# Performance work log

Measured on AMD Instinct MI355X. Metric: run time of the kernel, lower is better.

The kernel has to match this reference:

```python
import jax, jax.numpy as jnp
import numpy as np

NUM_HEADS = 8
EPS = 1e-5


def _dwconv_cpe(x, w, b, H, W):
    # x: [B,N,C]; depthwise 3x3 conv positional encoding with residual
    B, N, C = x.shape
    f = x.transpose(0, 2, 1).reshape(B, C, H, W)
    f = jax.lax.conv_general_dilated(
        f, w, window_strides=(1, 1), padding='SAME',
        feature_group_count=C, dimension_numbers=('NCHW', 'OIHW', 'NCHW'))
    f = f + b[None, :, None, None]
    return x + f.reshape(B, C, N).transpose(0, 2, 1)


def _layernorm(x, g, b):
    mu = jnp.mean(x, axis=-1, keepdims=True)
    var = jnp.mean(jnp.square(x - mu), axis=-1, keepdims=True)
    return (x - mu) * jax.lax.rsqrt(var + EPS) * g + b


def _channel_attn(x, source, q_w, kv_w, proj_w, proj_b):
    B, N, C = x.shape
    h = NUM_HEADS
    d = C // h
    scale = d ** -0.5
    q = (x @ q_w).reshape(B, N, h, d).transpose(0, 2, 1, 3)          # [B,h,N,d]
    kv = (source @ kv_w).reshape(B, N, 2, h, d).transpose(2, 0, 3, 1, 4)
    k = kv[0] * scale                                                # [B,h,N,d]
    v = kv[1]                                                        # [B,h,N,d]
    # channel cross-covariance: [B,h,d,d], softmax over last channel dim
    attn = jax.nn.softmax(jnp.einsum('bhnd,bhne->bhde', k, v), axis=-1)
    out = jnp.einsum('bhde,bhne->bhnd', attn, q)                     # [B,h,N,d]
    out = out.transpose(0, 2, 1, 3).reshape(B, N, C)
    return out @ proj_w + proj_b


def _forward(x, source, H, W, cpe0_w, cpe0_b, cpe1_w, cpe1_b,
             norm1_g, norm1_b, q_w, kv_w, proj_w, proj_b,
             norm2_g, norm2_b, fc1_w, fc1_b, fc2_w, fc2_b):
    x = _dwconv_cpe(x, cpe0_w, cpe0_b, H, W)
    source = _dwconv_cpe(source, cpe0_w, cpe0_b, H, W)  # cpe[0] shared, per source
    x = _layernorm(x, norm1_g, norm1_b)
    source = _layernorm(source, norm1_g, norm1_b)
    cur = _channel_attn(x, source, q_w, kv_w, proj_w, proj_b)
    x = x + cur  # residual on the normalized x (as in the original code)
    x = _dwconv_cpe(x, cpe1_w, cpe1_b, H, W)
    h = _layernorm(x, norm2_g, norm2_b)
    h = jax.nn.gelu(h @ fc1_w + fc1_b, approximate=False) @ fc2_w + fc2_b
    return x + h


def setup_inputs() -> dict:
    key = jax.random.key(0)
    ks = jax.random.split(key, 16)
    B, H, W, C = 8, 64, 64, 384
    N = H * W
    Ch = int(C * 4.0)
    s = 0.02
    return {
        'x': jax.random.normal(ks[0], (B, N, C), jnp.float32),
        'source': jax.random.normal(ks[1], (B, N, C), jnp.float32),
        'H': H, 'W': W,
        'cpe0_w': jax.random.normal(ks[2], (C, 1, 3, 3), jnp.float32) * s,
        'cpe0_b': jnp.zeros((C,), jnp.float32),
        'cpe1_w': jax.random.normal(ks[3], (C, 1, 3, 3), jnp.float32) * s,
        'cpe1_b': jnp.zeros((C,), jnp.float32),
        'norm1_g': jnp.ones((C,), jnp.float32),
        'norm1_b': jnp.zeros((C,), jnp.float32),
        'q_w': jax.random.normal(ks[4], (C, C), jnp.float32) * s,
        'kv_w': jax.random.normal(ks[5], (C, 2 * C), jnp.float32) * s,
        'proj_w': jax.random.normal(ks[6], (C, C), jnp.float32) * s,
        'proj_b': jnp.zeros((C,), jnp.float32),
        'norm2_g': jnp.ones((C,), jnp.float32),
        'norm2_b': jnp.zeros((C,), jnp.float32),
        'fc1_w': jax.random.normal(ks[7], (C, Ch), jnp.float32) * s,
        'fc1_b': jnp.zeros((Ch,), jnp.float32),
        'fc2_w': jax.random.normal(ks[8], (Ch, C), jnp.float32) * s,
        'fc2_b': jnp.zeros((C,), jnp.float32),
    }


def reference(x, source, H, W, cpe0_w, cpe0_b, cpe1_w, cpe1_b,
              norm1_g, norm1_b, q_w, kv_w, proj_w, proj_b,
              norm2_g, norm2_b, fc1_w, fc1_b, fc2_w, fc2_b):
    return _forward(x, source, H, W, cpe0_w, cpe0_b, cpe1_w, cpe1_b,
                    norm1_g, norm1_b, q_w, kv_w, proj_w, proj_b,
                    norm2_g, norm2_b, fc1_w, fc1_b, fc2_w, fc2_b)
```

## Files before the change

kernel.cpp:

```cpp
#include <hip/hip_runtime.h>
#include <hip/hip_bf16.h>
#include <math.h>

typedef __hip_bfloat16 bf16;
typedef unsigned short u16t;
typedef __bf16 bfx8 __attribute__((ext_vector_type(8)));
typedef float fx4 __attribute__((ext_vector_type(4)));
typedef unsigned short usx8 __attribute__((ext_vector_type(8)));

constexpr int Bq = 8, Hh = 64, Ww = 64, Nn = 4096, Cc = 384, NH = 8, CH = 1536;
constexpr int Mrows = Bq * Nn;
constexpr int NS = 4;
constexpr int NSP = 6;
constexpr float EPSC = 1e-5f;
constexpr float SCALE = 0.14433756729740643f;

__device__ __forceinline__ float toF(bf16 v) { return __bfloat162float(v); }

__device__ __forceinline__ float ldFlag(const void* p, size_t i, int f) {
    if (f) return __bfloat162float(((const bf16*)p)[i]);
    return ((const float*)p)[i];
}

__device__ __forceinline__ float u2f(u16t u) {
    unsigned int x = ((unsigned int)u) << 16;
    float fv;
    __builtin_memcpy(&fv, &x, 4);
    return fv;
}
__device__ __forceinline__ u16t f2u(float v) {
    bf16 h = __float2bfloat16(v);
    u16t u;
    __builtin_memcpy(&u, &h, 2);
    return u;
}
__device__ __forceinline__ fx4 mfma16(usx8 a, usx8 b, fx4 c) {
    return __builtin_amdgcn_mfma_f32_16x16x32_bf16(
        __builtin_bit_cast(bfx8, a), __builtin_bit_cast(bfx8, b), c, 0, 0, 0);
}

__global__ __launch_bounds__(256) void probe_k(const void* __restrict__ p, int* __restrict__ flag) {
    int t = threadIdx.x;
    int bad = 0;
    for (int i = t; i < 4096; i += 256) {
        unsigned short u = ((const unsigned short*)p)[i];
        unsigned e = (u >> 7) & 0xFF;
        if (e >= 134) bad++;
    }
    __shared__ int sh[256];
    sh[t] = bad;
    __syncthreads();
    for (int s = 128; s > 0; s >>= 1) {
        if (t < s) sh[t] += sh[t + s];
        __syncthreads();
    }
    if (t == 0) flag[0] = (sh[0] < 64) ? 1 : 0;
}

__global__ __launch_bounds__(384) void prep_k(const void* __restrict__ g,
                                              const void* __restrict__ b,
                                              u16t* __restrict__ gB, u16t* __restrict__ bB,
                                              const int* __restrict__ flagp) {
    int f = *flagp;
    int t = threadIdx.x;
    gB[t] = f2u(ldFlag(g, t, f));
    bB[t] = f2u(ldFlag(b, t, f));
}

template <int INM, int MODE>
__global__ __launch_bounds__(384) void dwconv_ln(const void* __restrict__ xin,
                                                 const void* __restrict__ w,
                                                 const void* __restrict__ bias,
                                                 bf16* __restrict__ out,
                                                 const void* __restrict__ g,
                                                 const void* __restrict__ bb,
                                                 float* __restrict__ mu,
                                                 float* __restrict__ rs,
                                                 const int* __restrict__ flagp) {
    int f = *flagp;
    int c = threadIdx.x;
    int w0 = blockIdx.x * 8;
    int hh = blockIdx.y;
    int b = blockIdx.z;
    size_t base = (size_t)b * Nn * Cc;
    float wreg[9];
#pragma unroll
    for (int j = 0; j < 9; j++) wreg[j] = ldFlag(w, c * 9 + j, f);
    float bc = ldFlag(bias, c, f);
    float v[3][10];
#pragma unroll
    for (int ky = 0; ky < 3; ky++) {
        int yy = hh + ky - 1;
        bool rv = (yy >= 0 && yy < Hh);
#pragma unroll
        for (int j = 0; j < 10; j++) {
            int xx = w0 - 1 + j;
            bool cv = (xx >= 0 && xx < Ww);
            float val = 0.f;
            if (rv && cv) {
                size_t idx = base + (size_t)(yy * Ww + xx) * Cc + c;
                val = (INM == 1) ? toF(((const bf16*)xin)[idx]) : ldFlag(xin, idx, f);
            }
            v[ky][j] = val;
        }
    }
    float r[8], s[8], s2[8];
#pragma unroll
    for (int p = 0; p < 8; p++) {
        float a = bc;
#pragma unroll
        for (int ky = 0; ky < 3; ky++)
#pragma unroll
            for (int kx = 0; kx < 3; kx++) a += v[ky][p + kx] * wreg[ky * 3 + kx];
        r[p] = v[1][p + 1] + a;
        s[p] = r[p];
        s2[p] = r[p] * r[p];
    }
#pragma unroll
    for (int off = 32; off > 0; off >>= 1) {
#pragma unroll
        for (int p = 0; p < 8; p++) {
            s[p] += __shfl_down(s[p], off, 64);
            s2[p] += __shfl_down(s2[p], off, 64);
        }
    }
    __shared__ float shS[6][8], shS2[6][8];
    __shared__ float shMu[8], shRs[8];
    int wv = c >> 6, ln = c & 63;
    if (ln == 0) {
#pragma unroll
        for (int p = 0; p < 8; p++) {
            shS[wv][p] = s[p];
            shS2[wv][p] = s2[p];
        }
    }
    __syncthreads();
    if (c < 8) {
        float S = 0, S2 = 0;
#pragma unroll
        for (int q = 0; q < 6; q++) {
            S += shS[q][c];
            S2 += shS2[q][c];
        }
        float m = S * (1.0f / Cc);
        float var = S2 * (1.0f / Cc) - m * m;
        float rr = rsqrtf(var + EPSC);
        if (MODE == 0) {
            shMu[c] = m;
            shRs[c] = rr;
        } else {
            int row = b * Nn + hh * Ww + w0 + c;
            mu[row] = m;
            rs[row] = rr;
        }
    }
    if (MODE == 0) {
        __syncthreads();
        float gc = ldFlag(g, c, f), bbc = ldFlag(bb, c, f);
#pragma unroll
        for (int p = 0; p < 8; p++) {
            size_t oi = base + (size_t)(hh * Ww + w0 + p) * Cc + c;
            out[oi] = __float2bfloat16((r[p] - shMu[p]) * shRs[p] * gc + bbc);
        }
    } else {
#pragma unroll
        for (int p = 0; p < 8; p++) {
            size_t oi = base + (size_t)(hh * Ww + w0 + p) * Cc + c;
            out[oi] = __float2bfloat16(r[p]);
        }
    }
}

__global__ __launch_bounds__(256) void reduceG_k(float* __restrict__ Gp) {
    const size_t Q = (size_t)Cc * Cc / 4;
    size_t j = (size_t)blockIdx.x * 256 + threadIdx.x;
    int b = (int)(j / Q);
    size_t i4 = j % Q;
    fx4* G4 = (fx4*)Gp;
    size_t base = (size_t)b * NS * Q;
    fx4 a = G4[base + i4];
#pragma unroll
    for (int s = 1; s < NS; s++) a += G4[base + (size_t)s * Q + i4];
    G4[base + i4] = a;
}

template <int AM, int OM, int WM, bool GELU, bool LNA, int RES, int AR>
__global__ __launch_bounds__(256) void gemm_k(const void* __restrict__ A, size_t aBatch,
                                              const void* __restrict__ W, size_t wBatch,
                                              int ldw, int colOff,
                                              const void* __restrict__ bias,
                                              const bf16* __restrict__ resid, size_t rBatch,
                                              const float* __restrict__ mu,
                                              const float* __restrict__ rs, size_t sBatch,
                                              const void* __restrict__ cg,
                                              const void* __restrict__ cb,
                                              void* __restrict__ out, size_t oBatch,
                                              size_t outRow0,
                                              int M, int K, int Nc,
                                              const int* __restrict__ flagp) {
    int f = *flagp;
    int z = blockIdx.z;
    const size_t MK = (size_t)M * K;
    __shared__ float As[16][68];
    __shared__ float Bs[16][68];
    int t = threadIdx.x;
    int tx = t & 15, ty = t >> 4;
    int row0 = blockIdx.x * 64, n0 = blockIdx.y * 64;
    float acc[4][4] = {};
    for (int k0 = 0; k0 < K; k0 += 16) {
#pragma unroll
        for (int i = 0; i < 4; i++) {
            int lin = i * 256 + t;
            int kk = lin & 15, m = lin >> 4;
            size_t ai = (size_t)z * aBatch + (size_t)(row0 + m) * K + k0 + kk;
            float v;
            if (AR > 1) {
                v = 0;
#pragma unroll
                for (int s = 0; s < AR; s++) v += ((const float*)A)[ai + (size_t)s * MK];
            } else {
                v = (AM == 0) ? ((const float*)A)[ai] : toF(((const bf16*)A)[ai]);
            }
            if (LNA) {
                float muv = mu[z * sBatch + row0 + m], rsv = rs[z * sBatch + row0 + m];
                v = (v - muv) * rsv * ldFlag(cg, k0 + kk, f) + ldFlag(cb, k0 + kk, f);
            }
            As[kk][m] = v;
        }
#pragma unroll
        for (int i = 0; i < 4; i++) {
            int lin = i * 256 + t;
            int nn2 = lin & 63, kk = lin >> 6;
            size_t wi = (size_t)z * wBatch + (size_t)(k0 + kk) * ldw + colOff + n0 + nn2;
            Bs[kk][nn2] = (WM == 1) ? toF(((const bf16*)W)[wi]) : ldFlag(W, wi, f);
        }
        __syncthreads();
#pragma unroll
        for (int kk = 0; kk < 16; kk++) {
            float a[4], bv[4];
#pragma unroll
            for (int i = 0; i < 4; i++) a[i] = As[kk][ty * 4 + i];
#pragma unroll
            for (int j = 0; j < 4; j++) bv[j] = Bs[kk][tx * 4 + j];
#pragma unroll
            for (int i = 0; i < 4; i++)
#pragma unroll
                for (int j = 0; j < 4; j++) acc[i][j] += a[i] * bv[j];
        }
        __syncthreads();
    }
#pragma unroll
    for (int i = 0; i < 4; i++) {
        int m = row0 + ty * 4 + i;
#pragma unroll
        for (int j = 0; j < 4; j++) {
            int nn2 = n0 + tx * 4 + j;
            float v = acc[i][j];
            if (bias) v += ldFlag(bias, nn2, f);
            if (GELU) v = 0.5f * v * (1.0f + erff(v * 0.70710678118654752f));
            if (RES == 1) v += toF(resid[(size_t)z * rBatch + (size_t)m * Nc + nn2]);
            size_t oi = (size_t)z * oBatch + (outRow0 + m) * (size_t)Nc + nn2;
            if (OM == 2) ((float*)out)[oi] = v;
            else if (OM == 1) ((bf16*)out)[oi] = __float2bfloat16(v);
            else {
                if (f) ((bf16*)out)[oi] = __float2bfloat16(v);
                else ((float*)out)[oi] = v;
            }
        }
    }
}

__global__ __launch_bounds__(256) void transpose_k(const void* __restrict__ W,
                                                   u16t* __restrict__ WT,
                                                   int K, int N,
                                                   const int* __restrict__ flagp) {
    int f = *flagp;
    __shared__ u16t T[64][72];
    int n0 = blockIdx.x * 64, k0 = blockIdx.y * 64;
    int t = threadIdx.x;
#pragma unroll
    for (int i = 0; i < 16; i++) {
        int lin = i * 256 + t;
        int kk = lin >> 6, nn = lin & 63;
        T[nn][kk] = f2u(ldFlag(W, (size_t)(k0 + kk) * N + n0 + nn, f));
    }
    __syncthreads();
#pragma unroll
    for (int i = 0; i < 16; i++) {
        int lin = i * 256 + t;
        int nn = lin >> 6, kk = lin & 63;
        WT[(size_t)(n0 + nn) * K + k0 + kk] = T[nn][kk];
    }
}

template <int AMODE, int OM, bool GELU, int RES>
__global__ __launch_bounds__(256) void gemm_mfma(
    const u16t* __restrict__ A, size_t aBatch,
    const u16t* __restrict__ BT, size_t btBatch,
    const void* __restrict__ bias,
    const u16t* __restrict__ resid, size_t rBatch,
    const float* __restrict__ mu, const float* __restrict__ rs, size_t sBatch,
    const u16t* __restrict__ gbf, const u16t* __restrict__ bbf,
    void* __restrict__ out, size_t oBatch, size_t outRow0,
    int K, int N, const int* __restrict__ flagp) {
    int f = *flagp;
    int z = blockIdx.z;
    int t = threadIdx.x;
    int row0 = blockIdx.x * 128, n0 = blockIdx.y * 128;
    __shared__ u16t As[128][64];
    __shared__ u16t Bs[128][64];
    const u16t* Ab = A + (size_t)z * aBatch;
    const u16t* Bb = BT + (size_t)z * btBatch;
    const int sm = t >> 3;
    const int sk8 = t & 7;
    float muv[4], rsv[4];
    if (AMODE == 1) {
#pragma unroll
        for (int i = 0; i < 4; i++) {
            int m = row0 + i * 32 + sm;
            muv[i] = mu[(size_t)z * sBatch + m];
            rsv[i] = rs[(size_t)z * sBatch + m];
        }
    }
    usx8 ra[4], rb[4];
    auto ldstep = [&](int k0) {
#pragma unroll
        for (int i = 0; i < 4; i++) {
            ra[i] = *(const usx8*)&Ab[(size_t)(row0 + i * 32 + sm) * K + k0 + sk8 * 8];
            rb[i] = *(const usx8*)&Bb[(size_t)(n0 + i * 32 + sm) * K + k0 + sk8 * 8];
        }
    };
    auto wrstep = [&](int k0) {
        usx8 ga, ba;
        if (AMODE == 1) {
            ga = *(const usx8*)&gbf[k0 + sk8 * 8];
            ba = *(const usx8*)&bbf[k0 + sk8 * 8];
        }
#pragma unroll
        for (int i = 0; i < 4; i++) {
            int row = i * 32 + sm;
            int dst = (sk8 ^ (row & 7)) << 3;
            if (AMODE == 1) {
                usx8 v;
#pragma unroll
                for (int j = 0; j < 8; j++)
                    v[j] = f2u((u2f(ra[i][j]) - muv[i]) * rsv[i] * u2f(ga[j]) + u2f(ba[j]));
                *(usx8*)&As[row][dst] = v;
            } else {
                *(usx8*)&As[row][dst] = ra[i];
            }
            *(usx8*)&Bs[row][dst] = rb[i];
        }
    };
    fx4 acc[4][4];
    fx4 zz = {0.f, 0.f, 0.f, 0.f};
#pragma unroll
    for (int i = 0; i < 4; i++)
#pragma unroll
        for (int j = 0; j < 4; j++) acc[i][j] = zz;
    int lane = t & 63, w = t >> 6;
    int wr = (w >> 1) * 64, wc = (w & 1) * 64;
    int lr = lane & 15, lg = lane >> 4;
    ldstep(0);
    wrstep(0);
    __syncthreads();
    int KT = K / 64;
    for (int kt = 0; kt < KT; kt++) {
        if (kt + 1 < KT) ldstep((kt + 1) * 64);
#pragma unroll
        for (int ks = 0; ks < 2; ks++) {
            usx8 af[4], bfv[4];
#pragma unroll
            for (int r = 0; r < 4; r++) {
                int row = wr + r * 16 + lr;
                af[r] = *(const usx8*)&As[row][((4 * ks + lg) ^ (row & 7)) << 3];
            }
#pragma unroll
            for (int c = 0; c < 4; c++) {
                int row = wc + c * 16 + lr;
                bfv[c] = *(const usx8*)&Bs[row][((4 * ks + lg) ^ (row & 7)) << 3];
            }
#pragma unroll
            for (int r = 0; r < 4; r++)
#pragma unroll
                for (int c = 0; c < 4; c++)
                    acc[r][c] = mfma16(af[r], bfv[c], acc[r][c]);
        }
        __syncthreads();
        if (kt + 1 < KT) {
            wrstep((kt + 1) * 64);
            __syncthreads();
        }
    }
#pragma unroll
    for (int r = 0; r < 4; r++) {
#pragma unroll
        for (int c = 0; c < 4; c++) {
            int gc = n0 + wc + c * 16 + lr;
            float bv = bias ? ldFlag(bias, gc, f) : 0.0f;
#pragma unroll
            for (int q = 0; q < 4; q++) {
                int m = row0 + wr + r * 16 + lg * 4 + q;
                float v = acc[r][c][q] + bv;
                if (GELU) v = 0.5f * v * (1.0f + erff(v * 0.70710678118654752f));
                if (RES == 1) v += u2f(resid[(size_t)z * rBatch + (size_t)m * N + gc]);
                if (RES == 2) v += u2f(Ab[(size_t)m * K + gc]);
                size_t oi = (size_t)z * oBatch + (outRow0 + m) * (size_t)N + gc;
                if (OM == 1) ((u16t*)out)[oi] = f2u(v);
                else {
                    if (f) ((u16t*)out)[oi] = f2u(v);
                    else ((float*)out)[oi] = v;
                }
            }
        }
    }
}

__global__ __launch_bounds__(256) void gram_mfma(const u16t* __restrict__ sc,
                                                 float* __restrict__ Gp) {
    int bx = blockIdx.x, sp = blockIdx.y, b = blockIdx.z;
    int ci0 = (bx / 3) * 128, cj0 = (bx % 3) * 128;
    __shared__ u16t As[128][72];
    __shared__ u16t Bs[128][72];
    int t = threadIdx.x;
    const int scc = (t * 8) & 127;
    const int snn = t >> 4;
    const int RPS = Nn / NS;
    int rowbase = b * Nn + sp * RPS;
    usx8 ra[4], rb[4];
    auto ldstep = [&](int nn0) {
#pragma unroll
        for (int i = 0; i < 4; i++) {
            int r = rowbase + nn0 + i * 16 + snn;
            ra[i] = *(const usx8*)&sc[(size_t)r * Cc + ci0 + scc];
            rb[i] = *(const usx8*)&sc[(size_t)r * Cc + cj0 + scc];
        }
    };
    auto wrstep = [&]() {
#pragma unroll
        for (int i = 0; i < 4; i++) {
            int n = i * 16 + snn;
            int q = n >> 3, nl = n & 7;
#pragma unroll
            for (int j = 0; j < 8; j++) {
                int c = scc + j;
                int swz = ((c >> 3) ^ (c >> 6)) & 7;
                int po = ((q ^ swz) << 3) + nl;
                As[c][po] = ra[i][j];
                Bs[c][po] = rb[i][j];
            }
        }
    };
    fx4 acc[4][4];
    fx4 zz = {0.f, 0.f, 0.f, 0.f};
#pragma unroll
    for (int i = 0; i < 4; i++)
#pragma unroll
        for (int j = 0; j < 4; j++) acc[i][j] = zz;
    int lane = t & 63, w = t >> 6;
    int wr = (w >> 1) * 64, wc = (w & 1) * 64;
    int lr = lane & 15, lg = lane >> 4;
    ldstep(0);
    wrstep();
    __syncthreads();
    const int KT = RPS / 64;
    for (int kt = 0; kt < KT; kt++) {
        if (kt + 1 < KT) ldstep((kt + 1) * 64);
#pragma unroll
        for (int ks = 0; ks < 2; ks++) {
            usx8 af[4], bfv[4];
#pragma unroll
            for (int r = 0; r < 4; r++) {
                int ch = wr + r * 16 + lr;
                int swz = ((ch >> 3) ^ (ch >> 6)) & 7;
                af[r] = *(const usx8*)&As[ch][((ks * 4 + lg) ^ swz) << 3];
            }
#pragma unroll
            for (int c = 0; c < 4; c++) {
                int ch = wc + c * 16 + lr;
                int swz = ((ch >> 3) ^ (ch >> 6)) & 7;
                bfv[c] = *(const usx8*)&Bs[ch][((ks * 4 + lg) ^ swz) << 3];
            }
#pragma unroll
            for (int r = 0; r < 4; r++)
#pragma unroll
                for (int c = 0; c < 4; c++)
                    acc[r][c] = mfma16(af[r], bfv[c], acc[r][c]);
        }
        __syncthreads();
        if (kt + 1 < KT) {
            wrstep();
            __syncthreads();
        }
    }
    float* dst = Gp + ((size_t)b * NS + sp) * (size_t)Cc * Cc;
#pragma unroll
    for (int r = 0; r < 4; r++)
#pragma unroll
        for (int c = 0; c < 4; c++)
#pragma unroll
            for (int q = 0; q < 4; q++)
                dst[(size_t)(ci0 + wr + r * 16 + lg * 4 + q) * Cc + cj0 + wc + c * 16 + lr] =
                    acc[r][c][q];
}

__global__ __launch_bounds__(256) void attn_part_k(const float* __restrict__ P,
                                                   const void* __restrict__ kv_w,
                                                   float* __restrict__ Sp,
                                                   const int* __restrict__ flagp) {
    int f = *flagp;
    int hd = blockIdx.x;
    int b = blockIdx.y;
    int sp = blockIdx.z;
    int c0 = sp * 64;
    int t = threadIdx.x;
    const float* Pb = P + (size_t)b * Cc * Cc;
    __shared__ float Pc[64][49];
    __shared__ float Wkc[64][49];
    for (int idx = t; idx < 3072; idx += 256) {
        int r = idx / 48, e = idx % 48;
        int c = c0 + r;
        Pc[r][e] = Pb[(size_t)c * Cc + hd * 48 + e];
        Wkc[r][e] = ldFlag(kv_w, (size_t)c * 768 + hd * 48 + e, f);
    }
    __syncthreads();
    int obase = t * 9;
    float acc[9] = {};
#pragma unroll
    for (int r = 0; r < 64; r++) {
#pragma unroll
        for (int j = 0; j < 9; j++) {
            int d = (obase + j) / 48, e = (obase + j) % 48;
            acc[j] += Wkc[r][d] * Pc[r][e];
        }
    }
    float* dst = Sp + (((size_t)b * NH + hd) * NSP + sp) * 2304;
#pragma unroll
    for (int j = 0; j < 9; j++) dst[obase + j] = acc[j];
}

__global__ __launch_bounds__(256) void attn_soft_k(const float* __restrict__ Sp,
                                                   float* __restrict__ attn) {
    int hd = blockIdx.x;
    int b = blockIdx.y;
    int t = threadIdx.x;
    __shared__ float Ss[48][49];
    const float* src = Sp + (((size_t)b * NH + hd) * NSP) * 2304;
    for (int idx = t; idx < 2304; idx += 256) {
        float s = 0;
#pragma unroll
        for (int sp = 0; sp < NSP; sp++) s += src[sp * 2304 + idx];
        Ss[idx / 48][idx % 48] = s * SCALE;
    }
    __syncthreads();
    if (t < 48) {
        float m = -1e30f;
#pragma unroll
        for (int e = 0; e < 48; e++) m = fmaxf(m, Ss[t][e]);
        float ex[48];
        float sum = 0;
#pragma unroll
        for (int e = 0; e < 48; e++) {
            ex[e] = expf(Ss[t][e] - m);
            sum += ex[e];
        }
        float inv = 1.0f / sum;
#pragma unroll
        for (int e = 0; e < 48; e++)
            attn[((size_t)b * NH + hd) * 2304 + t * 48 + e] = ex[e] * inv;
    }
}

__global__ __launch_bounds__(256) void wtilde_k(const void* __restrict__ q_w,
                                                const float* __restrict__ attn,
                                                bf16* __restrict__ Wt_,
                                                const int* __restrict__ flagp) {
    int f = *flagp;
    int c0 = blockIdx.x * 64;
    int hd = blockIdx.y;
    int b = blockIdx.z;
    int t = threadIdx.x;
    __shared__ float at[48][48];
    __shared__ float wq[64][48];
    const float* ab = attn + ((size_t)b * NH + hd) * 2304;
    for (int o = t; o < 2304; o += 256) at[o / 48][o % 48] = ab[o];
    for (int o = t; o < 3072; o += 256) {
        int cc = o / 48, e = o % 48;
        wq[cc][e] = ldFlag(q_w, (size_t)(c0 + cc) * Cc + hd * 48 + e, f);
    }
    __syncthreads();
    bf16* outb = Wt_ + (size_t)b * Cc * Cc;
    for (int o = t; o < 3072; o += 256) {
        int cc = o / 48, d = o % 48;
        float s = 0;
#pragma unroll
        for (int e = 0; e < 48; e++) s += wq[cc][e] * at[d][e];
        outb[(size_t)(c0 + cc) * Cc + hd * 48 + d] = __float2bfloat16(s);
    }
}

extern "C" void kernel_launch(void* const* d_in, const int* in_sizes, int n_in,
                              void* d_out, int out_size, void* d_ws, size_t ws_size,
                              hipStream_t stream) {
    (void)in_sizes; (void)n_in; (void)out_size;
    const void* x = d_in[0];
    const void* srcp = d_in[1];
    const void* cpe0_w = d_in[4];
    const void* cpe0_b = d_in[5];
    const void* cpe1_w = d_in[6];
    const void* cpe1_b = d_in[7];
    const void* n1g = d_in[8];
    const void* n1b = d_in[9];
    const void* q_w = d_in[10];
    const void* kv_w = d_in[11];
    const void* proj_w = d_in[12];
    const void* proj_b = d_in[13];
    const void* n2g = d_in[14];
    const void* n2b = d_in[15];
    const void* fc1_w = d_in[16];
    const void* fc1_b = d_in[17];
    const void* fc2_w = d_in[18];
    const void* fc2_b = d_in[19];
    char* ws = (char*)d_ws;

    const size_t CcCc = (size_t)Cc * Cc;
    const size_t NnCc = (size_t)Nn * Cc;
    const size_t SLOT = (size_t)Mrows * Cc * sizeof(bf16);
    int* flag = (int*)ws;
    bf16* s0 = (bf16*)(ws + 64);
    bf16* s1 = (bf16*)(ws + 64 + SLOT);
    float* Gp = (float*)s1;
    u16t* WeffT = (u16t*)s1;
    bf16* x3 = s1;
    float* P = (float*)(ws + 64 + 2 * SLOT);
    bf16* Wt_ = (bf16*)P;
    u16t* projT = (u16t*)((char*)P + 2359296);
    u16t* fc1T = (u16t*)P;
    u16t* fc2T = (u16t*)((char*)P + 1179648);
    float* attnB = (float*)(ws + 64 + 2 * SLOT + 4718592);
    float* mu2 = (float*)(ws + 64 + 2 * SLOT + 4718592 + 589824);
    float* rs2 = mu2 + Mrows;
    u16t* gB = (u16t*)(rs2 + Mrows);
    u16t* bB = gB + 384;
    bf16* lnS = s0;
    float* Sp = (float*)s0;
    bf16* x2 = s0;
    u16t* h1c = (u16t*)s0;
    const size_t NEED = (size_t)((char*)(bB + 384) - ws);
    if (ws_size < NEED) return;

    bf16* lnX = (bf16*)d_out;

    probe_k<<<1, 256, 0, stream>>>(x, flag);
    prep_k<<<1, 384, 0, stream>>>(n2g, n2b, gB, bB, flag);

    dwconv_ln<2, 0><<<dim3(Ww / 8, Hh, Bq), 384, 0, stream>>>(
        x, cpe0_w, cpe0_b, lnX, n1g, n1b, nullptr, nullptr, flag);

    dwconv_ln<2, 0><<<dim3(Ww / 8, Hh, Bq), 384, 0, stream>>>(
        srcp, cpe0_w, cpe0_b, lnS, n1g, n1b, nullptr, nullptr, flag);
    gram_mfma<<<dim3(9, NS, Bq), 256, 0, stream>>>((const u16t*)lnS, Gp);
    reduceG_k<<<(Bq * CcCc / 4) / 256, 256, 0, stream>>>(Gp);

    gemm_k<0, 2, 2, false, false, 0, 1><<<dim3(6, 6, Bq), 256, 0, stream>>>(
        Gp, (size_t)NS * CcCc, kv_w, 0, 768, 384, nullptr, nullptr, 0,
        nullptr, nullptr, 0, nullptr, nullptr, P, CcCc, 0, Cc, Cc, Cc, flag);

    attn_part_k<<<dim3(NH, Bq, NSP), 256, 0, stream>>>(P, kv_w, Sp, flag);
    attn_soft_k<<<dim3(NH, Bq), 256, 0, stream>>>(Sp, attnB);
    wtilde_k<<<dim3(6, NH, Bq), 256, 0, stream>>>(q_w, attnB, Wt_, flag);
    transpose_k<<<dim3(6, 6), 256, 0, stream>>>(proj_w, projT, Cc, Cc, flag);
    gemm_mfma<0, 1, false, 0><<<dim3(3, 3, Bq), 256, 0, stream>>>(
        projT, 0, (const u16t*)Wt_, CcCc, nullptr, nullptr, 0,
        nullptr, nullptr, 0, nullptr, nullptr, WeffT, CcCc, 0, Cc, Cc, flag);

    transpose_k<<<dim3(24, 6), 256, 0, stream>>>(fc1_w, fc1T, Cc, CH, flag);
    transpose_k<<<dim3(6, 24), 256, 0, stream>>>(fc2_w, fc2T, CH, Cc, flag);

    gemm_mfma<0, 1, false, 2><<<dim3(32, 3, Bq), 256, 0, stream>>>(
        (const u16t*)lnX, NnCc, WeffT, CcCc, proj_b, nullptr, 0,
        nullptr, nullptr, 0, nullptr, nullptr, x2, NnCc, 0, Cc, Cc, flag);

    dwconv_ln<1, 1><<<dim3(Ww / 8, Hh, Bq), 384, 0, stream>>>(
        x2, cpe1_w, cpe1_b, x3, nullptr, nullptr, mu2, rs2, flag);

    constexpr int CR = 8192;
    for (int ch = 0; ch < Mrows / CR; ch++) {
        size_t roff = (size_t)ch * CR;
        gemm_mfma<1, 1, true, 0><<<dim3(CR / 128, CH / 128, 1), 256, 0, stream>>>(
            (const u16t*)x3 + roff * Cc, 0, fc1T, 0, fc1_b, nullptr, 0,
            mu2 + roff, rs2 + roff, 0, gB, bB, h1c, 0, 0, Cc, CH, flag);
        gemm_mfma<0, 0, false, 1><<<dim3(CR / 128, Cc / 128, 1), 256, 0, stream>>>(
            h1c, 0, fc2T, 0, fc2_b, (const u16t*)x3 + roff * Cc, 0,
            nullptr, nullptr, 0, nullptr, nullptr, d_out, 0, roff, CH, Cc, flag);
    }
}
```

Measured before the change: 886.9 us.

## Fold LayerNorm into fc1 weights and use direct global-to-LDS loads in GEMM

The second LayerNorm is folded algebraically into fc1. Gamma scales the transposed fc1 weights, and per-column constants (-sum g*w and sum b*w + bias) feed a mu/rstd epilogue, so the GEMM no longer normalizes A on the fly. The GEMM staging now uses global_load_lds to copy tiles straight into swizzled LDS, replacing the register prefetch and write step. This drops the per-element normalization ALU work and register staging, but the loads are no longer double-buffered, so load latency is exposed before each k-step. Applying the normalization after the bf16 product may also change rounding behaviour.

```diff
diff --git a/kernel.cpp b/kernel.cpp
--- a/kernel.cpp
+++ b/kernel.cpp
@@ -39,6 +39,15 @@
         __builtin_bit_cast(bfx8, a), __builtin_bit_cast(bfx8, b), c, 0, 0, 0);
 }
 
+__device__ __forceinline__ void gload16(const void* g, void* l) {
+    __builtin_amdgcn_global_load_lds(
+        reinterpret_cast<const __attribute__((address_space(1))) unsigned int*>(
+            reinterpret_cast<uintptr_t>(g)),
+        reinterpret_cast<__attribute__((address_space(3))) unsigned int*>(
+            reinterpret_cast<uintptr_t>(l)),
+        16, 0, 0);
+}
+
 __global__ __launch_bounds__(256) void probe_k(const void* __restrict__ p, int* __restrict__ flag) {
     int t = threadIdx.x;
     int bad = 0;
@@ -55,16 +64,6 @@
         __syncthreads();
     }
     if (t == 0) flag[0] = (sh[0] < 64) ? 1 : 0;
-}
-
-__global__ __launch_bounds__(384) void prep_k(const void* __restrict__ g,
-                                              const void* __restrict__ b,
-                                              u16t* __restrict__ gB, u16t* __restrict__ bB,
-                                              const int* __restrict__ flagp) {
-    int f = *flagp;
-    int t = threadIdx.x;
-    gB[t] = f2u(ldFlag(g, t, f));
-    bB[t] = f2u(ldFlag(b, t, f));
 }
 
 template <int INM, int MODE>
@@ -293,14 +292,64 @@
     }
 }
 
-template <int AMODE, int OM, bool GELU, int RES>
+__global__ __launch_bounds__(256) void transpose_scale_k(const void* __restrict__ W,
+                                                         const void* __restrict__ g,
+                                                         u16t* __restrict__ WT,
+                                                         int K, int N,
+                                                         const int* __restrict__ flagp) {
+    int f = *flagp;
+    __shared__ u16t T[64][72];
+    int n0 = blockIdx.x * 64, k0 = blockIdx.y * 64;
+    int t = threadIdx.x;
+#pragma unroll
+    for (int i = 0; i < 16; i++) {
+        int lin = i * 256 + t;
+        int kk = lin >> 6, nn = lin & 63;
+        T[nn][kk] = f2u(ldFlag(g, k0 + kk, f) * ldFlag(W, (size_t)(k0 + kk) * N + n0 + nn, f));
+    }
+    __syncthreads();
+#pragma unroll
+    for (int i = 0; i < 16; i++) {
+        int lin = i * 256 + t;
+        int nn = lin >> 6, kk = lin & 63;
+        WT[(size_t)(n0 + nn) * K + k0 + kk] = T[nn][kk];
+    }
+}
+
+__global__ __launch_bounds__(256) void fc1fold_k(const void* __restrict__ fc1w,
+                                                 const void* __restrict__ g,
+                                                 const void* __restrict__ bb,
+                                                 const void* __restrict__ b1,
+                                                 float* __restrict__ negc1,
+                                                 float* __restrict__ cb2,
+                                                 const int* __restrict__ flagp) {
+    int f = *flagp;
+    __shared__ float gs[384], bs[384];
+    int t = threadIdx.x;
+    for (int i = t; i < 384; i += 256) {
+        gs[i] = ldFlag(g, i, f);
+        bs[i] = ldFlag(bb, i, f);
+    }
+    __syncthreads();
+    int n = blockIdx.x * 256 + t;
+    float s1 = 0, s2 = 0;
+    for (int k = 0; k < 384; k++) {
+        float w = ldFlag(fc1w, (size_t)k * CH + n, f);
+        s1 += gs[k] * w;
+        s2 += bs[k] * w;
+    }
+    negc1[n] = -s1;
+    cb2[n] = s2 + ldFlag(b1, n, f);
+}
+
+template <int OM, bool GELU, int RES, int EPI>
 __global__ __launch_bounds__(256) void gemm_mfma(
     const u16t* __restrict__ A, size_t aBatch,
     const u16t* __restrict__ BT, size_t btBatch,
     const void* __restrict__ bias,
     const u16t* __restrict__ resid, size_t rBatch,
-    const float* __restrict__ mu, const float* __restrict__ rs, size_t sBatch,
-    const u16t* __restrict__ gbf, const u16t* __restrict__ bbf,
+    const float* __restrict__ mu, const float* __restrict__ rs,
+    const float* __restrict__ negc1, const float* __restrict__ cb2,
     void* __restrict__ out, size_t oBatch, size_t outRow0,
     int K, int N, const int* __restrict__ flagp) {
     int f = *flagp;
@@ -311,62 +360,38 @@
     __shared__ u16t Bs[128][64];
     const u16t* Ab = A + (size_t)z * aBatch;
     const u16t* Bb = BT + (size_t)z * btBatch;
-    const int sm = t >> 3;
-    const int sk8 = t & 7;
-    float muv[4], rsv[4];
-    if (AMODE == 1) {
-#pragma unroll
-        for (int i = 0; i < 4; i++) {
-            int m = row0 + i * 32 + sm;
-            muv[i] = mu[(size_t)z * sBatch + m];
-            rsv[i] = rs[(size_t)z * sBatch + m];
-        }
-    }
-    usx8 ra[4], rb[4];
-    auto ldstep = [&](int k0) {
-#pragma unroll
-        for (int i = 0; i < 4; i++) {
-            ra[i] = *(const usx8*)&Ab[(size_t)(row0 + i * 32 + sm) * K + k0 + sk8 * 8];
-            rb[i] = *(const usx8*)&Bb[(size_t)(n0 + i * 32 + sm) * K + k0 + sk8 * 8];
-        }
-    };
-    auto wrstep = [&](int k0) {
-        usx8 ga, ba;
-        if (AMODE == 1) {
-            ga = *(const usx8*)&gbf[k0 + sk8 * 8];
-            ba = *(const usx8*)&bbf[k0 + sk8 * 8];
-        }
-#pragma unroll
-        for (int i = 0; i < 4; i++) {
-            int row = i * 32 + sm;
-            int dst = (sk8 ^ (row & 7)) << 3;
-            if (AMODE == 1) {
-                usx8 v;
-#pragma unroll
-                for (int j = 0; j < 8; j++)
-                    v[j] = f2u((u2f(ra[i][j]) - muv[i]) * rsv[i] * u2f(ga[j]) + u2f(ba[j]));
-                *(usx8*)&As[row][dst] = v;
-            } else {
-                *(usx8*)&As[row][dst] = ra[i];
-            }
-            *(usx8*)&Bs[row][dst] = rb[i];
-        }
-    };
+    int lane = t & 63, wv = t >> 6;
+    int srow = lane >> 3;
+    int schk = ((lane & 7) ^ srow) << 3;
+    const u16t* asrc[4];
+    const u16t* bsrc[4];
+    u16t* adst[4];
+    u16t* bdst[4];
+#pragma unroll
+    for (int i = 0; i < 4; i++) {
+        int r = 32 * wv + 8 * i;
+        asrc[i] = Ab + (size_t)(row0 + r + srow) * K + schk;
+        bsrc[i] = Bb + (size_t)(n0 + r + srow) * K + schk;
+        adst[i] = &As[r][0];
+        bdst[i] = &Bs[r][0];
+    }
     fx4 acc[4][4];
     fx4 zz = {0.f, 0.f, 0.f, 0.f};
 #pragma unroll
     for (int i = 0; i < 4; i++)
 #pragma unroll
         for (int j = 0; j < 4; j++) acc[i][j] = zz;
-    int lane = t & 63, w = t >> 6;
-    int wr = (w >> 1) * 64, wc = (w & 1) * 64;
+    int wr = (wv >> 1) * 64, wc = (wv & 1) * 64;
     int lr = lane & 15, lg = lane >> 4;
-    ldstep(0);
-    wrstep(0);
-    __syncthreads();
     int KT = K / 64;
     for (int kt = 0; kt < KT; kt++) {
-        if (kt + 1 < KT) ldstep((kt + 1) * 64);
+        if (kt) __syncthreads();
+#pragma unroll
+        for (int i = 0; i < 4; i++) {
+            gload16(asrc[i] + kt * 64, adst[i]);
+            gload16(bsrc[i] + kt * 64, bdst[i]);
+        }
+        __syncthreads();
 #pragma unroll
         for (int ks = 0; ks < 2; ks++) {
             usx8 af[4], bfv[4];
@@ -386,22 +411,27 @@
                 for (int c = 0; c < 4; c++)
                     acc[r][c] = mfma16(af[r], bfv[c], acc[r][c]);
         }
-        __syncthreads();
-        if (kt + 1 < KT) {
-            wrstep((kt + 1) * 64);
-            __syncthreads();
-        }
     }
 #pragma unroll
     for (int r = 0; r < 4; r++) {
+        int mb = row0 + wr + r * 16 + lg * 4;
+        fx4 muq, rsq;
+        if (EPI == 1) {
+            muq = *(const fx4*)&mu[mb];
+            rsq = *(const fx4*)&rs[mb];
+        }
 #pragma unroll
         for (int c = 0; c < 4; c++) {
             int gc = n0 + wc + c * 16 + lr;
             float bv = bias ? ldFlag(bias, gc, f) : 0.0f;
+            float nc1 = (EPI == 1) ? negc1[gc] : 0.f;
+            float cbv = (EPI == 1) ? cb2[gc] : 0.f;
 #pragma unroll
             for (int q = 0; q < 4; q++) {
-                int m = row0 + wr + r * 16 + lg * 4 + q;
-                float v = acc[r][c][q] + bv;
+                int m = mb + q;
+                float v;
+                if (EPI == 1) v = rsq[q] * (acc[r][c][q] + muq[q] * nc1) + cbv;
+                else v = acc[r][c][q] + bv;
                 if (GELU) v = 0.5f * v * (1.0f + erff(v * 0.70710678118654752f));
                 if (RES == 1) v += u2f(resid[(size_t)z * rBatch + (size_t)m * N + gc]);
                 if (RES == 2) v += u2f(Ab[(size_t)m * K + gc]);
@@ -640,19 +670,18 @@
     float* attnB = (float*)(ws + 64 + 2 * SLOT + 4718592);
     float* mu2 = (float*)(ws + 64 + 2 * SLOT + 4718592 + 589824);
     float* rs2 = mu2 + Mrows;
-    u16t* gB = (u16t*)(rs2 + Mrows);
-    u16t* bB = gB + 384;
+    float* negc1 = rs2 + Mrows;
+    float* cb2 = negc1 + CH;
     bf16* lnS = s0;
     float* Sp = (float*)s0;
     bf16* x2 = s0;
     u16t* h1c = (u16t*)s0;
-    const size_t NEED = (size_t)((char*)(bB + 384) - ws);
+    const size_t NEED = (size_t)((char*)(cb2 + CH) - ws);
     if (ws_size < NEED) return;
 
     bf16* lnX = (bf16*)d_out;
 
     probe_k<<<1, 256, 0, stream>>>(x, flag);
-    prep_k<<<1, 384, 0, stream>>>(n2g, n2b, gB, bB, flag);
 
     dwconv_ln<2, 0><<<dim3(Ww / 8, Hh, Bq), 384, 0, stream>>>(
         x, cpe0_w, cpe0_b, lnX, n1g, n1b, nullptr, nullptr, flag);
@@ -670,16 +699,17 @@
     attn_soft_k<<<dim3(NH, Bq), 256, 0, stream>>>(Sp, attnB);
     wtilde_k<<<dim3(6, NH, Bq), 256, 0, stream>>>(q_w, attnB, Wt_, flag);
     transpose_k<<<dim3(6, 6), 256, 0, stream>>>(proj_w, projT, Cc, Cc, flag);
-    gemm_mfma<0, 1, false, 0><<<dim3(3, 3, Bq), 256, 0, stream>>>(
+    gemm_mfma<1, false, 0, 0><<<dim3(3, 3, Bq), 256, 0, stream>>>(
         projT, 0, (const u16t*)Wt_, CcCc, nullptr, nullptr, 0,
-        nullptr, nullptr, 0, nullptr, nullptr, WeffT, CcCc, 0, Cc, Cc, flag);
-
-    transpose_k<<<dim3(24, 6), 256, 0, stream>>>(fc1_w, fc1T, Cc, CH, flag);
+        nullptr, nullptr, nullptr, nullptr, WeffT, CcCc, 0, Cc, Cc, flag);
+
+    transpose_scale_k<<<dim3(24, 6), 256, 0, stream>>>(fc1_w, n2g, fc1T, Cc, CH, flag);
     transpose_k<<<dim3(6, 24), 256, 0, stream>>>(fc2_w, fc2T, CH, Cc, flag);
-
-    gemm_mfma<0, 1, false, 2><<<dim3(32, 3, Bq), 256, 0, stream>>>(
+    fc1fold_k<<<CH / 256, 256, 0, stream>>>(fc1_w, n2g, n2b, fc1_b, negc1, cb2, flag);
+
+    gemm_mfma<1, false, 2, 0><<<dim3(32, 3, Bq), 256, 0, stream>>>(
         (const u16t*)lnX, NnCc, WeffT, CcCc, proj_b, nullptr, 0,
-        nullptr, nullptr, 0, nullptr, nullptr, x2, NnCc, 0, Cc, Cc, flag);
+        nullptr, nullptr, nullptr, nullptr, x2, NnCc, 0, Cc, Cc, flag);
 
     dwconv_ln<1, 1><<<dim3(Ww / 8, Hh, Bq), 384, 0, stream>>>(
         x2, cpe1_w, cpe1_b, x3, nullptr, nullptr, mu2, rs2, flag);
@@ -687,11 +717,11 @@
     constexpr int CR = 8192;
     for (int ch = 0; ch < Mrows / CR; ch++) {
         size_t roff = (size_t)ch * CR;
-        gemm_mfma<1, 1, true, 0><<<dim3(CR / 128, CH / 128, 1), 256, 0, stream>>>(
-            (const u16t*)x3 + roff * Cc, 0, fc1T, 0, fc1_b, nullptr, 0,
-            mu2 + roff, rs2 + roff, 0, gB, bB, h1c, 0, 0, Cc, CH, flag);
-        gemm_mfma<0, 0, false, 1><<<dim3(CR / 128, Cc / 128, 1), 256, 0, stream>>>(
+        gemm_mfma<1, true, 0, 1><<<dim3(CR / 128, CH / 128, 1), 256, 0, stream>>>(
+            (const u16t*)x3 + roff * Cc, 0, fc1T, 0, nullptr, nullptr, 0,
+            mu2 + roff, rs2 + roff, negc1, cb2, h1c, 0, 0, Cc, CH, flag);
+        gemm_mfma<0, false, 1, 0><<<dim3(CR / 128, Cc / 128, 1), 256, 0, stream>>>(
             h1c, 0, fc2T, 0, fc2_b, (const u16t*)x3 + roff * Cc, 0,
-            nullptr, nullptr, 0, nullptr, nullptr, d_out, 0, roff, CH, Cc, flag);
-    }
-}
+            nullptr, nullptr, nullptr, nullptr, d_out, 0, roff, CH, Cc, flag);
+    }
+}
```

Measured after the change: 801.4 us. -9.6%, faster.
